# Kernel optimization log

Measured on AMD Instinct MI355X. Metric: run time of the kernel, lower is better.

Reference implementation:

```python
import jax, jax.numpy as jnp
import numpy as np
from jax import lax

B, C, T = 8, 512, 2048
TEMP = 0.07
EPS = 1e-12


def setup_inputs() -> dict:
    key = jax.random.key(0)
    k1, k2, k3, k4 = jax.random.split(key, 4)
    x = jax.random.normal(k1, (B, C, T), dtype=jnp.float32)
    w_qkv = jax.random.normal(k2, (3 * C, C, 1), dtype=jnp.float32) * (1.0 / np.sqrt(C))
    w_dw = jax.random.normal(k3, (3 * C, 1, 3), dtype=jnp.float32) * (1.0 / np.sqrt(3))
    w_proj = jax.random.normal(k4, (C, C, 1), dtype=jnp.float32) * (1.0 / np.sqrt(C))
    return {"x": x, "w_qkv": w_qkv, "w_dw": w_dw, "w_proj": w_proj}


def _l2norm_ch(a):
    # F.normalize(a, dim=1): divide by L2 norm over channel dim, clamped at eps
    n = jnp.sqrt(jnp.sum(a * a, axis=1, keepdims=True))
    return a / jnp.maximum(n, EPS)


def reference(x, w_qkv, w_dw, w_proj):
    # 1x1 conv: [B,C,T] x [3C,C] -> [B,3C,T]
    qkv = jnp.einsum('bct,oc->bot', x, w_qkv[:, :, 0])
    # depthwise conv, kernel 3, padding 1, groups = 3C
    qkv = lax.conv_general_dilated(
        qkv, w_dw, window_strides=(1,), padding=[(1, 1)],
        dimension_numbers=('NCH', 'OIH', 'NCH'), feature_group_count=3 * C)
    q, k, v = jnp.split(qkv, 3, axis=1)  # each [B,C,T]
    q = _l2norm_ch(q)
    k = _l2norm_ch(k)
    # attn over tokens: [B,T,T]
    attn = jax.nn.softmax(jnp.einsum('bct,bcs->bts', q, k) / TEMP, axis=-1)
    out = jnp.einsum('bts,bcs->bct', attn, v)  # [B,C,T]
    return jnp.einsum('bct,oc->bot', out, w_proj[:, :, 0])
```

## Files before the change

### kernel.cpp

```cpp
#include <hip/hip_runtime.h>
#include <math.h>

static constexpr int B_ = 8, C_ = 512, T_ = 2048, C3_ = 1536;
static constexpr float INV_TEMP = 1.0f / 0.07f;

typedef __attribute__((ext_vector_type(8))) short short8;
typedef __attribute__((ext_vector_type(4))) float floatx4;

__device__ __forceinline__ float b2f(unsigned short u) {
  union { unsigned int i; float f; } v; v.i = ((unsigned int)u) << 16; return v.f;
}
__device__ __forceinline__ unsigned short f2b(float f) {
  union { float f; unsigned int i; } v; v.f = f;
  const unsigned int x = v.i;
  return (unsigned short)((x + 0x7FFFu + ((x >> 16) & 1u)) >> 16);
}
__device__ __forceinline__ void gld16(const unsigned short* g, unsigned short* l) {
  __builtin_amdgcn_global_load_lds(
      (const __attribute__((address_space(1))) void*)g,
      (__attribute__((address_space(3))) void*)l, 16, 0, 0);
}

template<bool OUT_BF16, int MODE, int MAP = 0>
__global__ __launch_bounds__(256)
void gemm_tn(const unsigned short* __restrict__ A, const unsigned short* __restrict__ B,
             void* __restrict__ Cout, int K, int lda, int ldb, int ldc,
             long long sA, long long sB, long long sC,
             const float* __restrict__ rs, const float* __restrict__ cs,
             float* __restrict__ denom, int rcStride, float scale)
{
  constexpr int NL = 4;

  int bz, m0, n0;
  if (MAP == 2) {
    const int id = blockIdx.x;
    bz = id & 7;
    const int r = id >> 3;
    m0 = (r >> 2) * 128; n0 = (r & 3) * 128;
  } else {
    bz = blockIdx.z;
    m0 = blockIdx.y * 128; n0 = blockIdx.x * 128;
  }
  A += (long long)bz * sA;
  B += (long long)bz * sB;
  if (MODE == 2) { rs += (long long)bz * rcStride; cs += (long long)bz * rcStride;
                   denom += (long long)bz * rcStride; }
  if (MODE == 3) { rs += (long long)bz * rcStride; }
  const int tid = threadIdx.x;
  const int w = tid >> 6, lane = tid & 63;
  const int wm = (w >> 1) * 64, wn = (w & 1) * 64;
  const int rl = lane & 15, qd = lane >> 4;

  __shared__ __align__(16) unsigned short As[3][128 * 32];
  __shared__ __align__(16) unsigned short Bs[3][128 * 32];

  const int sr = lane >> 2, sg = lane & 3;
  const int ml0 = 32 * w + sr, ml1 = ml0 + 16;
  const int q0 = sg ^ ((ml0 >> 1) & 3), q1 = sg ^ ((ml1 >> 1) & 3);
  const unsigned short* gA0 = A + (long long)(m0 + ml0) * lda + q0 * 8;
  const unsigned short* gA1 = A + (long long)(m0 + ml1) * lda + q1 * 8;
  const unsigned short* gB0 = B + (long long)(n0 + ml0) * ldb + q0 * 8;
  const unsigned short* gB1 = B + (long long)(n0 + ml1) * ldb + q1 * 8;

  int aoff[4], boff[4];
  #pragma unroll
  for (int i = 0; i < 4; ++i) {
    const int mr = wm + i * 16 + rl;
    aoff[i] = mr * 32 + ((qd ^ ((mr >> 1) & 3)) * 8);
    const int nr = wn + i * 16 + rl;
    boff[i] = nr * 32 + ((qd ^ ((nr >> 1) & 3)) * 8);
  }

  floatx4 acc[4][4];
  #pragma unroll
  for (int i = 0; i < 4; ++i)
    #pragma unroll
    for (int j = 0; j < 4; ++j) acc[i][j] = 0.0f;

  auto stage = [&](int t, int bf) {
    const int ko = t * 32;
    gld16(gA0 + ko, As[bf] + (32 * w) * 32);
    gld16(gA1 + ko, As[bf] + (32 * w + 16) * 32);
    gld16(gB0 + ko, Bs[bf] + (32 * w) * 32);
    gld16(gB1 + ko, Bs[bf] + (32 * w + 16) * 32);
  };
  auto compute = [&](int bf) {
    short8 fa[4], fb[4];
    #pragma unroll
    for (int i = 0; i < 4; ++i) fa[i] = *(const short8*)(As[bf] + aoff[i]);
    #pragma unroll
    for (int j = 0; j < 4; ++j) fb[j] = *(const short8*)(Bs[bf] + boff[j]);
    #pragma unroll
    for (int i = 0; i < 4; ++i)
      #pragma unroll
      for (int j = 0; j < 4; ++j)
        acc[i][j] = __builtin_amdgcn_mfma_f32_16x16x32_bf16(fa[i], fb[j], acc[i][j], 0, 0, 0);
  };

  const int niter = K >> 5;
  stage(0, 0);
  stage(1, 1);
  int buf = 0;
  for (int i = 0; i < niter - 1; ++i) {
    asm volatile("s_waitcnt vmcnt(%0)\n\ts_barrier" :: "i"(NL) : "memory");
    if (i + 2 < niter) {
      int nb = buf + 2; if (nb >= 3) nb -= 3;
      stage(i + 2, nb);
    }
    compute(buf);
    if (++buf == 3) buf = 0;
  }
  asm volatile("s_waitcnt vmcnt(0)\n\ts_barrier" ::: "memory");
  compute(buf);

  #pragma unroll
  for (int i = 0; i < 4; ++i) {
    #pragma unroll
    for (int r = 0; r < 4; ++r) {
      const int row = m0 + wm + i * 16 + qd * 4 + r;
      float rowf = 0.f;
      if (MODE == 2) rowf = rs[row] * scale;
      if (MODE == 3) rowf = 1.0f / rs[row];
      float rsum = 0.f;
      #pragma unroll
      for (int j = 0; j < 4; ++j) {
        const int col = n0 + wn + j * 16 + rl;
        float v = acc[i][j][r];
        if (MODE == 2) {
          const float s = v * rowf * cs[col];
          const unsigned short pb = f2b(__expf(s - scale));
          rsum += b2f(pb);
          ((unsigned short*)Cout)[(long long)bz * sC + (long long)row * ldc + col] = pb;
          continue;
        }
        if (MODE == 3) v *= rowf;
        const long long idx = (long long)bz * sC + (long long)row * ldc + col;
        if (OUT_BF16) ((unsigned short*)Cout)[idx] = f2b(v);
        else          ((float*)Cout)[idx] = v;
      }
      if (MODE == 2) {
        #pragma unroll
        for (int m = 1; m < 16; m <<= 1) rsum += __shfl_xor(rsum, m);
        if (rl == 0) atomicAdd(denom + row, rsum);
      }
    }
  }
}

template<bool OUT_BF16, int MODE>
__global__ __launch_bounds__(1024)
void gemm_tn1024p(const unsigned short* __restrict__ A, const unsigned short* __restrict__ B,
                  void* __restrict__ Cout, int K, int lda, int ldb, int ldc,
                  long long sA, long long sB, long long sC,
                  const float* __restrict__ rs, const float* __restrict__ cs,
                  float* __restrict__ denom, int rcStride, float scale)
{
  extern __shared__ unsigned short S[];

  const int id = blockIdx.x;
  const int bz = id & 7;
  const int rr = id >> 3;
  const int m0 = (rr >> 2) * 256;
  const int nb = (rr & 3) * 512;
  A += (long long)bz * sA;
  B += (long long)bz * sB;
  if (MODE == 2) { rs += (long long)bz * rcStride; cs += (long long)bz * rcStride;
                   denom += (long long)bz * rcStride; }
  const int tid = threadIdx.x;
  const int w = tid >> 6, lane = tid & 63;
  const int wm = (w >> 2) * 64, wn = (w & 3) * 64;
  const int rl = lane & 15, qd = lane >> 4;

  const int srow = w * 16 + (lane >> 2), sg = lane & 3;
  const int qa = sg ^ ((srow >> 1) & 3);
  const unsigned short* gA  = A + (long long)(m0 + srow) * lda + qa * 8;
  const unsigned short* gB0 = B + (long long)(nb + srow) * ldb + qa * 8;
  const unsigned short* gB1 = gB0 + (long long)256 * ldb;

  const int ar = wm + rl, br = wn + rl;
  const int aoff0 = ar * 32 + ((qd ^ ((ar >> 1) & 3)) * 8);
  const int boff0 = br * 32 + ((qd ^ ((br >> 1) & 3)) * 8);

  floatx4 acc[4][4];
  #pragma unroll
  for (int i = 0; i < 4; ++i)
    #pragma unroll
    for (int j = 0; j < 4; ++j) acc[i][j] = 0.0f;

  auto stage = [&](int t, int bf) {
    const int ko = (t & 15) * 32;
    const unsigned short* gb = (t < 16) ? gB0 : gB1;
    gld16(gA + ko, S + bf * 16384 + w * 512);
    gld16(gb + ko, S + bf * 16384 + 8192 + w * 512);
  };
  auto compute = [&](int bf) {
    short8 fa[4], fb[4];
    const unsigned short* pA = S + bf * 16384 + aoff0;
    const unsigned short* pB = S + bf * 16384 + 8192 + boff0;
    #pragma unroll
    for (int i = 0; i < 4; ++i) fa[i] = *(const short8*)(pA + i * 512);
    #pragma unroll
    for (int j = 0; j < 4; ++j) fb[j] = *(const short8*)(pB + j * 512);
    #pragma unroll
    for (int i = 0; i < 4; ++i)
      #pragma unroll
      for (int j = 0; j < 4; ++j)
        acc[i][j] = __builtin_amdgcn_mfma_f32_16x16x32_bf16(fa[i], fb[j], acc[i][j], 0, 0, 0);
  };
  auto epi = [&](int n0) {
    #pragma unroll
    for (int i = 0; i < 4; ++i) {
      #pragma unroll
      for (int r = 0; r < 4; ++r) {
        const int row = m0 + wm + i * 16 + qd * 4 + r;
        const float rowf = rs[row] * scale;
        float rsum = 0.f;
        #pragma unroll
        for (int j = 0; j < 4; ++j) {
          const int col = n0 + wn + j * 16 + rl;
          const float s = acc[i][j][r] * rowf * cs[col];
          const unsigned short pb = f2b(__expf(s - scale));
          rsum += b2f(pb);
          ((unsigned short*)Cout)[(long long)bz * sC + (long long)row * ldc + col] = pb;
        }
        #pragma unroll
        for (int m = 1; m < 16; m <<= 1) rsum += __shfl_xor(rsum, m);
        if (rl == 0) atomicAdd(denom + row, rsum);
      }
    }
    #pragma unroll
    for (int i = 0; i < 4; ++i)
      #pragma unroll
      for (int j = 0; j < 4; ++j) acc[i][j] = 0.0f;
  };

  stage(0, 0);
  stage(1, 1);
  int buf = 0;
  for (int i = 0; i < 31; ++i) {
    asm volatile("s_waitcnt vmcnt(2)\n\ts_barrier" ::: "memory");
    if (i + 2 < 32) {
      int nbuf = buf + 2; if (nbuf >= 3) nbuf -= 3;
      stage(i + 2, nbuf);
    }
    compute(buf);
    if (i == 15) epi(nb);
    if (++buf == 3) buf = 0;
  }
  asm volatile("s_waitcnt vmcnt(0)\n\ts_barrier" ::: "memory");
  compute(buf);
  epi(nb + 256);
}

__global__ __launch_bounds__(256)
void zero_f(float* __restrict__ p, int n)
{
  const int i = blockIdx.x * 256 + threadIdx.x;
  if (i < n) p[i] = 0.f;
}

__global__ __launch_bounds__(256)
void fin_inv(float* __restrict__ p, int n)
{
  const int i = blockIdx.x * 256 + threadIdx.x;
  if (i < n) p[i] = 1.f / fmaxf(sqrtf(p[i]), 1e-12f);
}

__global__ __launch_bounds__(256)
void conv_xT(const float* __restrict__ x, unsigned short* __restrict__ xT)
{
  const int b = blockIdx.z, t0 = blockIdx.x * 64, c0 = blockIdx.y * 64;
  const int tid = threadIdx.x;
  __shared__ float tile[64][65];
  const float* src = x + (long long)b * C_ * T_;
  const int cy = tid >> 2, g = tid & 3;
  const float* sp = src + (long long)(c0 + cy) * T_ + t0 + 16 * g;
  #pragma unroll
  for (int i = 0; i < 4; ++i) {
    const float4 v = *(const float4*)(sp + 4 * i);
    tile[cy][16 * g + 4 * i + 0] = v.x;
    tile[cy][16 * g + 4 * i + 1] = v.y;
    tile[cy][16 * g + 4 * i + 2] = v.z;
    tile[cy][16 * g + 4 * i + 3] = v.w;
  }
  __syncthreads();
  const int tl = tid >> 2, cg = tid & 3;
  short8 o0, o1;
  #pragma unroll
  for (int i = 0; i < 8; ++i) {
    o0[i] = (short)f2b(tile[16 * cg + i][tl]);
    o1[i] = (short)f2b(tile[16 * cg + 8 + i][tl]);
  }
  unsigned short* dst = xT + (long long)b * T_ * C_ + (long long)(t0 + tl) * C_ + c0 + 16 * cg;
  *(short8*)dst = o0;
  *(short8*)(dst + 8) = o1;
}

__global__ __launch_bounds__(256)
void conv_bf(const float* __restrict__ in, unsigned short* __restrict__ out, int n)
{
  const int i = blockIdx.x * 256 + threadIdx.x;
  if (i < n) out[i] = f2b(in[i]);
}

__global__ __launch_bounds__(256)
void dw_qkv_v2(const unsigned short* __restrict__ qkv, const float* __restrict__ wdw,
               unsigned short* __restrict__ qT, unsigned short* __restrict__ kT,
               unsigned short* __restrict__ vout,
               float* __restrict__ sq_q, float* __restrict__ sq_k)
{
  const int bz = blockIdx.z, b = bz / 3, p = bz % 3;
  const int t0 = blockIdx.x * 64, c0 = blockIdx.y * 64;
  const int tid = threadIdx.x;
  __shared__ unsigned short tin[64][80];
  __shared__ float tout[64][65];
  const int chb = b * C3_ + p * C_;

  #pragma unroll
  for (int s = 0; s < 2; ++s) {
    const int idx = tid + s * 256;
    const int cy = idx >> 3, g = idx & 7;
    *(short8*)&tin[cy][8 + 8 * g] =
        *(const short8*)(qkv + (long long)(chb + c0 + cy) * T_ + t0 + 8 * g);
  }
  if (tid < 64) {
    tin[tid][7] = (t0 > 0) ? qkv[(long long)(chb + c0 + tid) * T_ + t0 - 1]
                           : (unsigned short)0;
  } else if (tid < 128) {
    const int cy = tid - 64;
    tin[cy][72] = (t0 + 64 < T_) ? qkv[(long long)(chb + c0 + cy) * T_ + t0 + 64]
                                 : (unsigned short)0;
  }
  __syncthreads();

  const int cy = tid >> 2, tg = tid & 3;
  const float* wp = wdw + (p * C_ + c0 + cy) * 3;
  const float w0 = wp[0], w1 = wp[1], w2 = wp[2];

  if (p == 2) {
    short8 o0, o1;
    #pragma unroll
    for (int i = 0; i < 16; ++i) {
      const int j = 16 * tg + i;
      const float v = fmaf(w0, b2f(tin[cy][7 + j]),
                      fmaf(w1, b2f(tin[cy][8 + j]), w2 * b2f(tin[cy][9 + j])));
      if (i < 8) o0[i] = (short)f2b(v); else o1[i - 8] = (short)f2b(v);
    }
    unsigned short* d = vout + (long long)(b * C_ + c0 + cy) * T_ + t0 + 16 * tg;
    *(short8*)d = o0;
    *(short8*)(d + 8) = o1;
    return;
  }

  #pragma unroll
  for (int i = 0; i < 16; ++i) {
    const int j = 16 * tg + i;
    tout[j][cy] = fmaf(w0, b2f(tin[cy][7 + j]),
                  fmaf(w1, b2f(tin[cy][8 + j]), w2 * b2f(tin[cy][9 + j])));
  }
  __syncthreads();

  unsigned short* dst = (p == 0 ? qT : kT) + (long long)b * T_ * C_;
  float* sq = (p == 0 ? sq_q : sq_k) + (long long)b * T_;
  #pragma unroll
  for (int s = 0; s < 2; ++s) {
    const int idx = tid + s * 256;
    const int tl = idx >> 3, cl = idx & 7;
    short8 o;
    float ssq = 0.f;
    #pragma unroll
    for (int i = 0; i < 8; ++i) {
      const unsigned short ub = f2b(tout[tl][8 * cl + i]);
      o[i] = (short)ub;
      const float fv = b2f(ub);
      ssq = fmaf(fv, fv, ssq);
    }
    *(short8*)(dst + (long long)(t0 + tl) * C_ + c0 + 8 * cl) = o;
    #pragma unroll
    for (int m = 1; m < 8; m <<= 1) ssq += __shfl_xor(ssq, m);
    if (cl == 0) atomicAdd(sq + t0 + tl, ssq);
  }
}

extern "C" void kernel_launch(void* const* d_in, const int* in_sizes, int n_in,
                              void* d_out, int out_size, void* d_ws, size_t ws_size,
                              hipStream_t stream)
{
  const float* x      = (const float*)d_in[0];
  const float* w_qkv  = (const float*)d_in[1];
  const float* w_dw   = (const float*)d_in[2];
  const float* w_proj = (const float*)d_in[3];
  float* out = (float*)d_out;

  static int attr_done = 0;
  if (!attr_done) {
    hipFuncSetAttribute((const void*)&gemm_tn1024p<true, 2>,
                        hipFuncAttributeMaxDynamicSharedMemorySize, 98304);
    attr_done = 1;
  }

  char* base = (char*)d_ws;
  unsigned short* xT      = (unsigned short*)base;
  unsigned short* wqkv_bf = (unsigned short*)(base + 16777216);
  unsigned short* av_t    = (unsigned short*)base;
  char* p = base + 67108864;
  unsigned short* qT = (unsigned short*)p; p += 16777216;
  unsigned short* kT = (unsigned short*)p; p += 16777216;
  unsigned short* vb = (unsigned short*)p; p += 16777216;
  unsigned short* attn   = (unsigned short*)p;
  unsigned short* qkv_bf = (unsigned short*)p;
  p += 67108864;
  unsigned short* wproj_bf = (unsigned short*)p; p += 524288;
  float* inv_nq = (float*)p; p += 65536;
  float* inv_nk = (float*)p; p += 65536;
  float* denom  = (float*)p;

  const long long TC = (long long)T_ * C_, TT = (long long)T_ * T_;

  conv_xT<<<dim3(T_ / 64, C_ / 64, B_), 256, 0, stream>>>(x, xT);
  conv_bf<<<(C3_ * C_) / 256, 256, 0, stream>>>(w_qkv, wqkv_bf, C3_ * C_);
  conv_bf<<<(C_ * C_) / 256, 256, 0, stream>>>(w_proj, wproj_bf, C_ * C_);
  zero_f<<<(3 * B_ * T_) / 256, 256, 0, stream>>>(inv_nq, 3 * B_ * T_);

  gemm_tn<true, 0><<<dim3(16, 12, B_), 256, 0, stream>>>(
      wqkv_bf, xT, qkv_bf, C_, C_, C_, T_,
      0LL, TC, (long long)C3_ * T_, nullptr, nullptr, nullptr, 0, 1.f);

  dw_qkv_v2<<<dim3(T_ / 64, C_ / 64, B_ * 3), 256, 0, stream>>>(
      qkv_bf, w_dw, qT, kT, vb, inv_nq, inv_nk);
  fin_inv<<<(2 * B_ * T_) / 256, 256, 0, stream>>>(inv_nq, 2 * B_ * T_);

  gemm_tn1024p<true, 2><<<dim3(32 * B_, 1, 1), 1024, 98304, stream>>>(
      qT, kT, attn, C_, C_, C_, T_,
      TC, TC, TT, inv_nq, inv_nk, denom, T_, INV_TEMP);

  gemm_tn<true, 3, 2><<<dim3(64 * B_, 1, 1), 256, 0, stream>>>(
      attn, vb, av_t, T_, T_, T_, C_,
      TT, (long long)C_ * T_, TC, denom, nullptr, nullptr, T_, 1.f);

  gemm_tn<false, 0><<<dim3(16, 4, B_), 256, 0, stream>>>(
      wproj_bf, av_t, out, C_, C_, C_, T_,
      0LL, TC, (long long)C_ * T_, nullptr, nullptr, nullptr, 0, 1.f);
}
```

Measured before the change: 277.6 us.

## Replace 1024-thread QK^T kernel with 512-thread 128x256 tile kernel

```diff
diff --git a/kernel.cpp b/kernel.cpp
--- a/kernel.cpp
+++ b/kernel.cpp
@@ -147,39 +147,47 @@
   }
 }
 
-template<bool OUT_BF16, int MODE>
-__global__ __launch_bounds__(1024)
-void gemm_tn1024p(const unsigned short* __restrict__ A, const unsigned short* __restrict__ B,
-                  void* __restrict__ Cout, int K, int lda, int ldb, int ldc,
-                  long long sA, long long sB, long long sC,
-                  const float* __restrict__ rs, const float* __restrict__ cs,
-                  float* __restrict__ denom, int rcStride, float scale)
+__global__ __launch_bounds__(512)
+void gemm_attn8(const unsigned short* __restrict__ A, const unsigned short* __restrict__ B,
+                unsigned short* __restrict__ Cout, int K, int lda, int ldb, int ldc,
+                long long sA, long long sB, long long sC,
+                const float* __restrict__ rs, const float* __restrict__ cs,
+                float* __restrict__ denom, int rcStride, float scale)
 {
   extern __shared__ unsigned short S[];
 
   const int id = blockIdx.x;
   const int bz = id & 7;
-  const int rr = id >> 3;
-  const int m0 = (rr >> 2) * 256;
-  const int nb = (rr & 3) * 512;
+  const int r = id >> 3;
+  const int m0 = (r >> 3) * 128, n0 = (r & 7) * 256;
   A += (long long)bz * sA;
   B += (long long)bz * sB;
-  if (MODE == 2) { rs += (long long)bz * rcStride; cs += (long long)bz * rcStride;
-                   denom += (long long)bz * rcStride; }
+  rs += (long long)bz * rcStride; cs += (long long)bz * rcStride;
+  denom += (long long)bz * rcStride;
   const int tid = threadIdx.x;
   const int w = tid >> 6, lane = tid & 63;
   const int wm = (w >> 2) * 64, wn = (w & 3) * 64;
   const int rl = lane & 15, qd = lane >> 4;
 
-  const int srow = w * 16 + (lane >> 2), sg = lane & 3;
-  const int qa = sg ^ ((srow >> 1) & 3);
-  const unsigned short* gA  = A + (long long)(m0 + srow) * lda + qa * 8;
-  const unsigned short* gB0 = B + (long long)(nb + srow) * ldb + qa * 8;
-  const unsigned short* gB1 = gB0 + (long long)256 * ldb;
-
-  const int ar = wm + rl, br = wn + rl;
-  const int aoff0 = ar * 32 + ((qd ^ ((ar >> 1) & 3)) * 8);
-  const int boff0 = br * 32 + ((qd ^ ((br >> 1) & 3)) * 8);
+  const int srw = tid >> 2, sg = tid & 3;
+  const int qa  = sg ^ ((srw >> 1) & 3);
+  const int brw1 = 128 + srw;
+  const int qb1 = sg ^ ((brw1 >> 1) & 3);
+  const unsigned short* gA  = A + (long long)(m0 + srw) * lda + qa * 8;
+  const unsigned short* gB0 = B + (long long)(n0 + srw) * ldb + qa * 8;
+  const unsigned short* gB1 = B + (long long)(n0 + brw1) * ldb + qb1 * 8;
+  unsigned short* dA  = S + srw * 32 + sg * 8;
+  unsigned short* dB0 = S + 12288 + srw * 32 + sg * 8;
+  unsigned short* dB1 = S + 12288 + brw1 * 32 + sg * 8;
+
+  int aoff[4], boff[4];
+  #pragma unroll
+  for (int i = 0; i < 4; ++i) {
+    const int mr = wm + i * 16 + rl;
+    aoff[i] = mr * 32 + ((qd ^ ((mr >> 1) & 3)) * 8);
+    const int nr = wn + i * 16 + rl;
+    boff[i] = 12288 + nr * 32 + ((qd ^ ((nr >> 1) & 3)) * 8);
+  }
 
   floatx4 acc[4][4];
   #pragma unroll
@@ -188,68 +196,65 @@
     for (int j = 0; j < 4; ++j) acc[i][j] = 0.0f;
 
   auto stage = [&](int t, int bf) {
-    const int ko = (t & 15) * 32;
-    const unsigned short* gb = (t < 16) ? gB0 : gB1;
-    gld16(gA + ko, S + bf * 16384 + w * 512);
-    gld16(gb + ko, S + bf * 16384 + 8192 + w * 512);
+    const int ko = t * 32;
+    gld16(gA + ko,  dA  + bf * 4096);
+    gld16(gB0 + ko, dB0 + bf * 8192);
+    gld16(gB1 + ko, dB1 + bf * 8192);
   };
   auto compute = [&](int bf) {
     short8 fa[4], fb[4];
-    const unsigned short* pA = S + bf * 16384 + aoff0;
-    const unsigned short* pB = S + bf * 16384 + 8192 + boff0;
-    #pragma unroll
-    for (int i = 0; i < 4; ++i) fa[i] = *(const short8*)(pA + i * 512);
-    #pragma unroll
-    for (int j = 0; j < 4; ++j) fb[j] = *(const short8*)(pB + j * 512);
+    const unsigned short* pA = S + bf * 4096;
+    const unsigned short* pB = S + bf * 8192;
+    #pragma unroll
+    for (int i = 0; i < 4; ++i) fa[i] = *(const short8*)(pA + aoff[i]);
+    #pragma unroll
+    for (int j = 0; j < 4; ++j) fb[j] = *(const short8*)(pB + boff[j]);
     #pragma unroll
     for (int i = 0; i < 4; ++i)
       #pragma unroll
       for (int j = 0; j < 4; ++j)
         acc[i][j] = __builtin_amdgcn_mfma_f32_16x16x32_bf16(fa[i], fb[j], acc[i][j], 0, 0, 0);
   };
-  auto epi = [&](int n0) {
-    #pragma unroll
-    for (int i = 0; i < 4; ++i) {
-      #pragma unroll
-      for (int r = 0; r < 4; ++r) {
-        const int row = m0 + wm + i * 16 + qd * 4 + r;
-        const float rowf = rs[row] * scale;
-        float rsum = 0.f;
-        #pragma unroll
-        for (int j = 0; j < 4; ++j) {
-          const int col = n0 + wn + j * 16 + rl;
-          const float s = acc[i][j][r] * rowf * cs[col];
-          const unsigned short pb = f2b(__expf(s - scale));
-          rsum += b2f(pb);
-          ((unsigned short*)Cout)[(long long)bz * sC + (long long)row * ldc + col] = pb;
-        }
-        #pragma unroll
-        for (int m = 1; m < 16; m <<= 1) rsum += __shfl_xor(rsum, m);
-        if (rl == 0) atomicAdd(denom + row, rsum);
-      }
-    }
-    #pragma unroll
-    for (int i = 0; i < 4; ++i)
-      #pragma unroll
-      for (int j = 0; j < 4; ++j) acc[i][j] = 0.0f;
-  };
-
+
+  const int niter = K >> 5;
   stage(0, 0);
   stage(1, 1);
   int buf = 0;
-  for (int i = 0; i < 31; ++i) {
-    asm volatile("s_waitcnt vmcnt(2)\n\ts_barrier" ::: "memory");
-    if (i + 2 < 32) {
-      int nbuf = buf + 2; if (nbuf >= 3) nbuf -= 3;
-      stage(i + 2, nbuf);
+  for (int i = 0; i < niter - 1; ++i) {
+    asm volatile("s_waitcnt vmcnt(3)\n\ts_barrier" ::: "memory");
+    if (i + 2 < niter) {
+      int nb = buf + 2; if (nb >= 3) nb -= 3;
+      stage(i + 2, nb);
     }
     compute(buf);
-    if (i == 15) epi(nb);
     if (++buf == 3) buf = 0;
   }
   asm volatile("s_waitcnt vmcnt(0)\n\ts_barrier" ::: "memory");
   compute(buf);
-  epi(nb + 256);
+
+  float cf4[4];
+  #pragma unroll
+  for (int j = 0; j < 4; ++j) cf4[j] = cs[n0 + wn + j * 16 + rl];
+  #pragma unroll
+  for (int i = 0; i < 4; ++i) {
+    #pragma unroll
+    for (int rr = 0; rr < 4; ++rr) {
+      const int row = m0 + wm + i * 16 + qd * 4 + rr;
+      const float rowf = rs[row] * scale;
+      float rsum = 0.f;
+      #pragma unroll
+      for (int j = 0; j < 4; ++j) {
+        const int col = n0 + wn + j * 16 + rl;
+        const float s = acc[i][j][rr] * rowf * cf4[j];
+        const unsigned short pb = f2b(__expf(s - scale));
+        rsum += b2f(pb);
+        Cout[(long long)bz * sC + (long long)row * ldc + col] = pb;
+      }
+      #pragma unroll
+      for (int m = 1; m < 16; m <<= 1) rsum += __shfl_xor(rsum, m);
+      if (rl == 0) atomicAdd(denom + row, rsum);
+    }
+  }
 }
 
 __global__ __launch_bounds__(256)
@@ -394,8 +399,8 @@
 
   static int attr_done = 0;
   if (!attr_done) {
-    hipFuncSetAttribute((const void*)&gemm_tn1024p<true, 2>,
-                        hipFuncAttributeMaxDynamicSharedMemorySize, 98304);
+    hipFuncSetAttribute((const void*)&gemm_attn8,
+                        hipFuncAttributeMaxDynamicSharedMemorySize, 73728);
     attr_done = 1;
   }
 
@@ -430,7 +435,7 @@
       qkv_bf, w_dw, qT, kT, vb, inv_nq, inv_nk);
   fin_inv<<<(2 * B_ * T_) / 256, 256, 0, stream>>>(inv_nq, 2 * B_ * T_);
 
-  gemm_tn1024p<true, 2><<<dim3(32 * B_, 1, 1), 1024, 98304, stream>>>(
+  gemm_attn8<<<dim3(128 * B_, 1, 1), 512, 73728, stream>>>(
       qT, kT, attn, C_, C_, C_, T_,
       TC, TC, TT, inv_nq, inv_nk, denom, T_, INV_TEMP);
 
```

After: 275.8 us. Within noise of the previous version (-0.6%).
